# Performance work log

Measured on AMD Instinct MI355X. Metric: run time of the kernel, lower is better.

The kernel has to match this reference:

```python
import jax, jax.numpy as jnp
import numpy as np

B, R, S, D, K = 4096, 49, 50, 512, 100

def setup_inputs() -> dict:
    key = jax.random.key(0)
    ks = jax.random.split(key, 10)
    return {
        "ifeature": jax.random.normal(ks[0], (B, R, D), dtype=jnp.float32),
        "tfeature_h": jax.random.normal(ks[1], (B, S, D), dtype=jnp.float32),
        "w_Vi_0": jax.random.normal(ks[2], (D, K), dtype=jnp.float32) * 0.05,
        "w_Vt_0": jax.random.normal(ks[3], (D, K), dtype=jnp.float32) * 0.05,
        "w_Pi_0": jax.random.normal(ks[4], (2 * K, 1), dtype=jnp.float32) * 0.05,
        "b_Pi_0": jnp.zeros((R,), dtype=jnp.float32),
        "w_Vi_1": jax.random.normal(ks[5], (D, K), dtype=jnp.float32) * 0.05,
        "w_Vt_1": jax.random.normal(ks[6], (D, K), dtype=jnp.float32) * 0.05,
        "w_Pi_1": jax.random.normal(ks[7], (2 * K, 1), dtype=jnp.float32) * 0.05,
        "b_Pi_1": jnp.zeros((S,), dtype=jnp.float32),
    }

def reference(ifeature, tfeature_h, w_Vi_0, w_Vt_0, w_Pi_0, b_Pi_0,
              w_Vi_1, w_Vt_1, w_Pi_1, b_Pi_1):
    # ---- pass 0: attend over image regions, conditioned on mean text feature
    tfeature = jnp.mean(tfeature_h, axis=1)                      # [B, D]
    wVi0 = jnp.einsum('brd,dk->brk', ifeature, w_Vi_0)           # [B, R, K]
    wVt0 = (tfeature @ w_Vt_0)[:, None, :]                       # [B, 1, K] -> broadcast over R
    Hi = jnp.tanh(jnp.concatenate(
        [wVi0, jnp.broadcast_to(wVt0, wVi0.shape)], axis=-1))    # [B, R, 2K]
    scores_i = jnp.squeeze(Hi @ w_Pi_0, axis=-1) + b_Pi_0        # [B, R]
    Pi = jax.nn.softmax(scores_i, axis=-1)                       # [B, R]
    Vi = jnp.einsum('br,brd->bd', Pi, ifeature)                  # [B, D]
    # ---- pass 1: attend over text positions, conditioned on attended image
    wVi1 = (Vi @ w_Vi_1)[:, None, :]                             # [B, 1, K]
    wVt1 = jnp.einsum('bsd,dk->bsk', tfeature_h, w_Vt_1)         # [B, S, K]
    Ht = jnp.tanh(jnp.concatenate(
        [jnp.broadcast_to(wVi1, wVt1.shape), wVt1], axis=-1))    # [B, S, 2K]
    scores_t = jnp.squeeze(Ht @ w_Pi_1, axis=-1) + b_Pi_1        # [B, S]
    Pt = jax.nn.softmax(scores_t, axis=-1)                       # [B, S]
    Vt = jnp.einsum('bs,bsd->bd', Pt, tfeature_h)                # [B, D]
    return Vi + Vt
```

## Files before the change

### kernel.cpp

```cpp
#include <hip/hip_runtime.h>
#include <math.h>

#define NB 4096
#define NR 49
#define NS 50
#define ND 512
#define NK 100
#define NT 7
#define KSTEPS 16
#define CHUNK_KS 8
#define FRAGS (NT * KSTEPS * 64 * 8)

typedef __attribute__((ext_vector_type(8))) short short8;
typedef __attribute__((ext_vector_type(4))) float f32x4;

__device__ __forceinline__ unsigned short f32_bf16(float f) {
    union { float f; unsigned u; } x; x.f = f;
    return (unsigned short)((x.u + 0x7fffu + ((x.u >> 16) & 1u)) >> 16);
}
__device__ __forceinline__ unsigned cvt_pk_bf16(float lo, float hi) {
    unsigned r;
    asm("v_cvt_pk_bf16_f32 %0, %1, %2" : "=v"(r) : "v"(lo), "v"(hi));
    return r;
}
__device__ __forceinline__ float fast_tanh(float x) {
    const float ax = fabsf(x);
    const float e = __expf(2.f * ax);
    const float r = 1.f - 2.f / (e + 1.f);
    return copysignf(r, x);
}

__global__ void preswz_kernel(const float* __restrict__ w0, const float* __restrict__ w1,
                              unsigned short* __restrict__ ws)
{
    const int l  = threadIdx.x;
    const int gk = blockIdx.x & 15;
    const int t  = blockIdx.x >> 4;
    const int m  = blockIdx.y;
    const float* W = m ? w1 : w0;
    const int col = t * 16 + (l & 15);
    const int k0  = gk * 32 + (l >> 4) * 8;
    unsigned short* o = ws + (size_t)m * FRAGS + ((size_t)(t * 16 + gk) * 64 + l) * 8;
#pragma unroll
    for (int j = 0; j < 8; ++j) {
        float v = (col < NK) ? W[(size_t)(k0 + j) * NK + col] : 0.f;
        o[j] = f32_bf16(v);
    }
}

struct SM {
    short buf[NS * 256];
    float part[NT][64];
    float P[64];
};

__global__ __launch_bounds__(512, 4) void coattn_main(
    const float* __restrict__ ifeat, const float* __restrict__ tfeat,
    const float* __restrict__ wPi0, const float* __restrict__ bPi0,
    const float* __restrict__ wPi1, const float* __restrict__ bPi1,
    const unsigned short* __restrict__ wsW, float* __restrict__ out)
{
    __shared__ SM sm;
    const int pass = blockIdx.x & 1;
    const int b    = blockIdx.x >> 1;
    const int tid  = threadIdx.x;

    const float* feat = pass ? (tfeat + (size_t)b * NS * ND) : (ifeat + (size_t)b * NR * ND);
    const int nrows  = pass ? NS : NR;
    const int nclamp = nrows - 1;
    const unsigned short* wsR = wsW + (size_t)pass * FRAGS;
    const float* wPiRow = pass ? (wPi1 + NK) : wPi0;
    const float* bvec   = pass ? bPi1 : bPi0;

    const int lane = tid & 63, wid = tid >> 6;
    const int colg = lane & 15, g = lane >> 4;

    const f32x4 zero4 = {0.f, 0.f, 0.f, 0.f};
    f32x4 acc[4] = {zero4, zero4, zero4, zero4};

    int arow_[4], rswz_[4];
#pragma unroll
    for (int rt = 0; rt < 4; ++rt) {
        const int r0 = rt * 16 + colg;
        arow_[rt] = (r0 < nclamp) ? r0 : nclamp;
        rswz_[rt] = arow_[rt] & 7;
    }

    const int nitems = nrows * 32;

    for (int chunk = 0; chunk < 2; ++chunk) {
        __syncthreads();
        for (int it = tid; it < nitems; it += 512) {
            const int r = it >> 5, c = it & 31;
            const float* p = feat + (r << 9) + (chunk << 8) + (c << 3);
            const float4 a  = *reinterpret_cast<const float4*>(p);
            const float4 b4 = *reinterpret_cast<const float4*>(p + 4);
            uint4 v;
            v.x = cvt_pk_bf16(a.x, a.y);   v.y = cvt_pk_bf16(a.z, a.w);
            v.z = cvt_pk_bf16(b4.x, b4.y); v.w = cvt_pk_bf16(b4.z, b4.w);
            *reinterpret_cast<uint4*>(&sm.buf[(r << 8) + ((c ^ (r & 7)) << 3)]) = v;
        }
        __syncthreads();

        if (wid < NT) {
            const unsigned short* wl = wsR
                + ((size_t)(wid * KSTEPS + chunk * CHUNK_KS) * 64 + lane) * 8;
#pragma unroll
            for (int ks = 0; ks < CHUNK_KS; ++ks) {
                const short8 w = *reinterpret_cast<const short8*>(wl + ks * 512);
                const int q0 = (ks << 2) + g;
#pragma unroll
                for (int rt = 0; rt < 4; ++rt) {
                    const short8 a = *reinterpret_cast<const short8*>(
                        &sm.buf[(arow_[rt] << 8) + ((q0 ^ rswz_[rt]) << 3)]);
                    acc[rt] = __builtin_amdgcn_mfma_f32_16x16x32_bf16(a, w, acc[rt], 0, 0, 0);
                }
            }
        }
    }

    if (wid < NT) {
        const int col = wid * 16 + colg;
        const float w = (col < NK) ? wPiRow[col] : 0.f;
        float sp[4][4];
#pragma unroll
        for (int rt = 0; rt < 4; ++rt)
#pragma unroll
            for (int i = 0; i < 4; ++i)
                sp[rt][i] = fast_tanh(acc[rt][i]) * w;
#pragma unroll
        for (int off = 1; off < 16; off <<= 1)
#pragma unroll
            for (int rt = 0; rt < 4; ++rt)
#pragma unroll
                for (int i = 0; i < 4; ++i)
                    sp[rt][i] += __shfl_xor(sp[rt][i], off);
        if (colg == 0) {
#pragma unroll
            for (int rt = 0; rt < 4; ++rt)
#pragma unroll
                for (int i = 0; i < 4; ++i)
                    sm.part[wid][rt * 16 + g * 4 + i] = sp[rt][i];
        }
    }
    __syncthreads();

    if (tid < 64) {
        float v = (tid < nrows) ? bvec[tid] : 0.f;
#pragma unroll
        for (int w = 0; w < NT; ++w) v += sm.part[w][tid];
        v = (tid < nrows) ? v : -3.0e38f;
        float mx = v;
#pragma unroll
        for (int off = 32; off; off >>= 1) mx = fmaxf(mx, __shfl_xor(mx, off));
        const float e = (tid < nrows) ? __expf(v - mx) : 0.f;
        float su = e;
#pragma unroll
        for (int off = 32; off; off >>= 1) su += __shfl_xor(su, off);
        sm.P[tid] = e / su;
    }
    __syncthreads();

    {
        float v = 0.f;
        const float* fp = feat + tid;
        for (int r = 0; r < nrows; ++r) v += sm.P[r] * fp[r << 9];
        atomicAdd(&out[(size_t)b * ND + tid], v);
    }
}

extern "C" void kernel_launch(void* const* d_in, const int* in_sizes, int n_in,
                              void* d_out, int out_size, void* d_ws, size_t ws_size,
                              hipStream_t stream) {
    const float* ifeat = (const float*)d_in[0];
    const float* tfeat = (const float*)d_in[1];
    const float* wVi0  = (const float*)d_in[2];
    const float* wPi0  = (const float*)d_in[4];
    const float* bPi0  = (const float*)d_in[5];
    const float* wVt1  = (const float*)d_in[7];
    const float* wPi1  = (const float*)d_in[8];
    const float* bPi1  = (const float*)d_in[9];
    float* outp = (float*)d_out;
    unsigned short* wsW = (unsigned short*)d_ws;

    hipMemsetAsync(outp, 0, (size_t)NB * ND * sizeof(float), stream);
    hipLaunchKernelGGL(preswz_kernel, dim3(NT * KSTEPS, 2), dim3(64), 0, stream,
                       wVi0, wVt1, wsW);
    hipLaunchKernelGGL(coattn_main, dim3(2 * NB), dim3(512), 0, stream,
                       ifeat, tfeat, wPi0, bPi0, wPi1, bPi1, wsW, outp);
}
```

Baseline: 306.4 us.

## Fuse both attention passes per block and reuse staged bf16 rows for weighted sum

After: 316.4 us. 3.3% more time.

```diff
diff --git a/kernel.cpp b/kernel.cpp
--- a/kernel.cpp
+++ b/kernel.cpp
@@ -8,7 +8,6 @@
 #define NK 100
 #define NT 7
 #define KSTEPS 16
-#define CHUNK_KS 8
 #define FRAGS (NT * KSTEPS * 64 * 8)
 
 typedef __attribute__((ext_vector_type(8))) short short8;
@@ -17,6 +16,10 @@
 __device__ __forceinline__ unsigned short f32_bf16(float f) {
     union { float f; unsigned u; } x; x.f = f;
     return (unsigned short)((x.u + 0x7fffu + ((x.u >> 16) & 1u)) >> 16);
+}
+__device__ __forceinline__ float bf16_f32(unsigned short h) {
+    union { unsigned u; float f; } x; x.u = ((unsigned)h) << 16;
+    return x.f;
 }
 __device__ __forceinline__ unsigned cvt_pk_bf16(float lo, float hi) {
     unsigned r;
@@ -49,123 +52,122 @@
 }
 
 struct SM {
-    short buf[NS * 256];
+    short buf[NS * ND];
     float part[NT][64];
     float P[64];
 };
 
-__global__ __launch_bounds__(512, 4) void coattn_main(
+__global__ __launch_bounds__(512, 6) void coattn_main(
     const float* __restrict__ ifeat, const float* __restrict__ tfeat,
     const float* __restrict__ wPi0, const float* __restrict__ bPi0,
     const float* __restrict__ wPi1, const float* __restrict__ bPi1,
     const unsigned short* __restrict__ wsW, float* __restrict__ out)
 {
     __shared__ SM sm;
-    const int pass = blockIdx.x & 1;
-    const int b    = blockIdx.x >> 1;
-    const int tid  = threadIdx.x;
-
-    const float* feat = pass ? (tfeat + (size_t)b * NS * ND) : (ifeat + (size_t)b * NR * ND);
-    const int nrows  = pass ? NS : NR;
-    const int nclamp = nrows - 1;
-    const unsigned short* wsR = wsW + (size_t)pass * FRAGS;
-    const float* wPiRow = pass ? (wPi1 + NK) : wPi0;
-    const float* bvec   = pass ? bPi1 : bPi0;
-
+    const int b = blockIdx.x, tid = threadIdx.x;
     const int lane = tid & 63, wid = tid >> 6;
     const int colg = lane & 15, g = lane >> 4;
+    const int wch = tid >> 3, wlo = tid & 7;
 
-    const f32x4 zero4 = {0.f, 0.f, 0.f, 0.f};
-    f32x4 acc[4] = {zero4, zero4, zero4, zero4};
+    float vi = 0.f;
 
-    int arow_[4], rswz_[4];
-#pragma unroll
-    for (int rt = 0; rt < 4; ++rt) {
-        const int r0 = rt * 16 + colg;
-        arow_[rt] = (r0 < nclamp) ? r0 : nclamp;
-        rswz_[rt] = arow_[rt] & 7;
-    }
+    for (int pass = 0; pass < 2; ++pass) {
+        const float* feat = pass ? (tfeat + (size_t)b * NS * ND)
+                                 : (ifeat + (size_t)b * NR * ND);
+        const int nrows  = pass ? NS : NR;
+        const int nclamp = nrows - 1;
+        const unsigned short* wsR = wsW + (size_t)pass * FRAGS;
+        const float* wPiRow = pass ? (wPi1 + NK) : wPi0;
+        const float* bvec   = pass ? bPi1 : bPi0;
 
-    const int nitems = nrows * 32;
-
-    for (int chunk = 0; chunk < 2; ++chunk) {
-        __syncthreads();
+        const int nitems = nrows * 64;
         for (int it = tid; it < nitems; it += 512) {
-            const int r = it >> 5, c = it & 31;
-            const float* p = feat + (r << 9) + (chunk << 8) + (c << 3);
+            const int r = it >> 6, c = it & 63;
+            const float* p = feat + (r << 9) + (c << 3);
             const float4 a  = *reinterpret_cast<const float4*>(p);
             const float4 b4 = *reinterpret_cast<const float4*>(p + 4);
             uint4 v;
             v.x = cvt_pk_bf16(a.x, a.y);   v.y = cvt_pk_bf16(a.z, a.w);
             v.z = cvt_pk_bf16(b4.x, b4.y); v.w = cvt_pk_bf16(b4.z, b4.w);
-            *reinterpret_cast<uint4*>(&sm.buf[(r << 8) + ((c ^ (r & 7)) << 3)]) = v;
+            *reinterpret_cast<uint4*>(&sm.buf[(r << 9) + ((c ^ (r & 7)) << 3)]) = v;
         }
         __syncthreads();
 
         if (wid < NT) {
-            const unsigned short* wl = wsR
-                + ((size_t)(wid * KSTEPS + chunk * CHUNK_KS) * 64 + lane) * 8;
+            int arow_[4], rswz_[4];
 #pragma unroll
-            for (int ks = 0; ks < CHUNK_KS; ++ks) {
+            for (int rt = 0; rt < 4; ++rt) {
+                const int r0 = rt * 16 + colg;
+                arow_[rt] = (r0 < nclamp) ? r0 : nclamp;
+                rswz_[rt] = arow_[rt] & 7;
+            }
+            const f32x4 zero4 = {0.f, 0.f, 0.f, 0.f};
+            f32x4 acc[4] = {zero4, zero4, zero4, zero4};
+            const unsigned short* wl = wsR + ((size_t)wid * KSTEPS * 64 + lane) * 8;
+#pragma unroll
+            for (int ks = 0; ks < KSTEPS; ++ks) {
                 const short8 w = *reinterpret_cast<const short8*>(wl + ks * 512);
                 const int q0 = (ks << 2) + g;
 #pragma unroll
                 for (int rt = 0; rt < 4; ++rt) {
                     const short8 a = *reinterpret_cast<const short8*>(
-                        &sm.buf[(arow_[rt] << 8) + ((q0 ^ rswz_[rt]) << 3)]);
+                        &sm.buf[(arow_[rt] << 9) + ((q0 ^ rswz_[rt]) << 3)]);
                     acc[rt] = __builtin_amdgcn_mfma_f32_16x16x32_bf16(a, w, acc[rt], 0, 0, 0);
                 }
             }
-        }
-    }
 
-    if (wid < NT) {
-        const int col = wid * 16 + colg;
-        const float w = (col < NK) ? wPiRow[col] : 0.f;
-        float sp[4][4];
-#pragma unroll
-        for (int rt = 0; rt < 4; ++rt)
-#pragma unroll
-            for (int i = 0; i < 4; ++i)
-                sp[rt][i] = fast_tanh(acc[rt][i]) * w;
-#pragma unroll
-        for (int off = 1; off < 16; off <<= 1)
+            const int col = wid * 16 + colg;
+            const float w = (col < NK) ? wPiRow[col] : 0.f;
+            float sp[4][4];
 #pragma unroll
             for (int rt = 0; rt < 4; ++rt)
 #pragma unroll
                 for (int i = 0; i < 4; ++i)
-                    sp[rt][i] += __shfl_xor(sp[rt][i], off);
-        if (colg == 0) {
+                    sp[rt][i] = fast_tanh(acc[rt][i]) * w;
 #pragma unroll
-            for (int rt = 0; rt < 4; ++rt)
+            for (int off = 1; off < 16; off <<= 1)
 #pragma unroll
-                for (int i = 0; i < 4; ++i)
-                    sm.part[wid][rt * 16 + g * 4 + i] = sp[rt][i];
+                for (int rt = 0; rt < 4; ++rt)
+#pragma unroll
+                    for (int i = 0; i < 4; ++i)
+                        sp[rt][i] += __shfl_xor(sp[rt][i], off);
+            if (colg == 0) {
+#pragma unroll
+                for (int rt = 0; rt < 4; ++rt)
+#pragma unroll
+                    for (int i = 0; i < 4; ++i)
+                        sm.part[wid][rt * 16 + g * 4 + i] = sp[rt][i];
+            }
         }
-    }
-    __syncthreads();
+        __syncthreads();
 
-    if (tid < 64) {
-        float v = (tid < nrows) ? bvec[tid] : 0.f;
+        if (tid < 64) {
+            float v = (tid < nrows) ? bvec[tid] : 0.f;
 #pragma unroll
-        for (int w = 0; w < NT; ++w) v += sm.part[w][tid];
-        v = (tid < nrows) ? v : -3.0e38f;
-        float mx = v;
+            for (int w = 0; w < NT; ++w) v += sm.part[w][tid];
+            v = (tid < nrows) ? v : -3.0e38f;
+            float mx = v;
 #pragma unroll
-        for (int off = 32; off; off >>= 1) mx = fmaxf(mx, __shfl_xor(mx, off));
-        const float e = (tid < nrows) ? __expf(v - mx) : 0.f;
-        float su = e;
+            for (int off = 32; off; off >>= 1) mx = fmaxf(mx, __shfl_xor(mx, off));
+            const float e = (tid < nrows) ? __expf(v - mx) : 0.f;
+            float su = e;
 #pragma unroll
-        for (int off = 32; off; off >>= 1) su += __shfl_xor(su, off);
-        sm.P[tid] = e / su;
-    }
-    __syncthreads();
+            for (int off = 32; off; off >>= 1) su += __shfl_xor(su, off);
+            sm.P[tid] = e / su;
+        }
+        __syncthreads();
 
-    {
-        float v = 0.f;
-        const float* fp = feat + tid;
-        for (int r = 0; r < nrows; ++r) v += sm.P[r] * fp[r << 9];
-        atomicAdd(&out[(size_t)b * ND + tid], v);
+        {
+            float v = 0.f;
+            for (int r = 0; r < nrows; ++r) {
+                const unsigned short u = (unsigned short)
+                    sm.buf[(r << 9) + ((wch ^ (r & 7)) << 3) + wlo];
+                v += sm.P[r] * bf16_f32(u);
+            }
+            if (pass == 0) vi = v;
+            else out[(size_t)b * ND + tid] = vi + v;
+        }
+        __syncthreads();
     }
 }
 
@@ -183,9 +185,8 @@
     float* outp = (float*)d_out;
     unsigned short* wsW = (unsigned short*)d_ws;
 
-    hipMemsetAsync(outp, 0, (size_t)NB * ND * sizeof(float), stream);
     hipLaunchKernelGGL(preswz_kernel, dim3(NT * KSTEPS, 2), dim3(64), 0, stream,
                        wVi0, wVt1, wsW);
-    hipLaunchKernelGGL(coattn_main, dim3(2 * NB), dim3(512), 0, stream,
+    hipLaunchKernelGGL(coattn_main, dim3(NB), dim3(512), 0, stream,
                        ifeat, tfeat, wPi0, bPi0, wPi1, bPi1, wsW, outp);
 }
```

## Double-buffer fp32 tiles via direct global-to-LDS loads and rebalance waves

Applied to the files above, without the earlier changes.

New measurement: 308.8 us. Within noise of the previous version (+0.8%).

```diff
diff --git a/kernel.cpp b/kernel.cpp
--- a/kernel.cpp
+++ b/kernel.cpp
@@ -8,7 +8,6 @@
 #define NK 100
 #define NT 7
 #define KSTEPS 16
-#define CHUNK_KS 8
 #define FRAGS (NT * KSTEPS * 64 * 8)
 
 typedef __attribute__((ext_vector_type(8))) short short8;
@@ -29,6 +28,14 @@
     const float r = 1.f - 2.f / (e + 1.f);
     return copysignf(r, x);
 }
+__device__ __forceinline__ void load_lds16(const float* g, float* l) {
+    __builtin_amdgcn_global_load_lds(
+        (const __attribute__((address_space(1))) unsigned int*)(const void*)g,
+        (__attribute__((address_space(3))) unsigned int*)(void*)l, 16, 0, 0);
+}
+#define FENCE() asm volatile("" ::: "memory")
+#define BARR()  do { FENCE(); __builtin_amdgcn_s_barrier(); FENCE(); } while (0)
+#define WAITV(N) asm volatile("s_waitcnt vmcnt(" #N ")" ::: "memory")
 
 __global__ void preswz_kernel(const float* __restrict__ w0, const float* __restrict__ w1,
                               unsigned short* __restrict__ ws)
@@ -49,8 +56,9 @@
 }
 
 struct SM {
-    short buf[NS * 256];
-    float part[NT][64];
+    float bufA[50 * 128];
+    float bufB[50 * 128];
+    float part[8][64];
     float P[64];
 };
 
@@ -74,81 +82,122 @@
 
     const int lane = tid & 63, wid = tid >> 6;
     const int colg = lane & 15, g = lane >> 4;
-
-    const f32x4 zero4 = {0.f, 0.f, 0.f, 0.f};
-    f32x4 acc[4] = {zero4, zero4, zero4, zero4};
-
-    int arow_[4], rswz_[4];
-#pragma unroll
-    for (int rt = 0; rt < 4; ++rt) {
-        const int r0 = rt * 16 + colg;
-        arow_[rt] = (r0 < nclamp) ? r0 : nclamp;
-        rswz_[rt] = arow_[rt] & 7;
-    }
-
-    const int nitems = nrows * 32;
-
-    for (int chunk = 0; chunk < 2; ++chunk) {
-        __syncthreads();
-        for (int it = tid; it < nitems; it += 512) {
-            const int r = it >> 5, c = it & 31;
-            const float* p = feat + (r << 9) + (chunk << 8) + (c << 3);
-            const float4 a  = *reinterpret_cast<const float4*>(p);
-            const float4 b4 = *reinterpret_cast<const float4*>(p + 4);
-            uint4 v;
-            v.x = cvt_pk_bf16(a.x, a.y);   v.y = cvt_pk_bf16(a.z, a.w);
-            v.z = cvt_pk_bf16(b4.x, b4.y); v.w = cvt_pk_bf16(b4.z, b4.w);
-            *reinterpret_cast<uint4*>(&sm.buf[(r << 8) + ((c ^ (r & 7)) << 3)]) = v;
+    const int q  = wid >> 1;
+    const int mh = wid & 1;
+    const int t0 = q * 2;
+    const int two = (q < 3);
+
+    int arow_[2], aswz_[2];
+#pragma unroll
+    for (int rl = 0; rl < 2; ++rl) {
+        const int r0 = (mh * 2 + rl) * 16 + colg;
+        arow_[rl] = (r0 < nclamp) ? r0 : nclamp;
+        aswz_[rl] = arow_[rl] & 7;
+    }
+    const unsigned short* wl0 = wsR + ((size_t)t0 * 16 * 64 + lane) * 8;
+    const unsigned short* wl1 = wl0 + (size_t)16 * 64 * 8;
+
+#define ISSUE(CP, BUF)                                                          \
+    do {                                                                        \
+        _Pragma("unroll") for (int s = 0; s < 3; ++s) {                         \
+            const int j = wid + (s << 3);                                       \
+            const int row = 2 * j + (lane >> 5);                                \
+            const int grow = (row < nrows) ? row : nclamp;                      \
+            const int c16 = lane & 31;                                          \
+            load_lds16(feat + (grow << 9) + ((CP) << 7) + ((c16 ^ (row & 7)) << 2), \
+                       sm.BUF + j * 256);                                       \
+        }                                                                       \
+        if (wid == 0) {                                                         \
+            const int row = 48 + (lane >> 5);                                   \
+            const int grow = (row < nrows) ? row : nclamp;                      \
+            const int c16 = lane & 31;                                          \
+            load_lds16(feat + (grow << 9) + ((CP) << 7) + ((c16 ^ (row & 7)) << 2), \
+                       sm.BUF + 24 * 256);                                      \
+        }                                                                       \
+    } while (0)
+#define WAITC() do { if (wid == 0) { WAITV(4); } else { WAITV(3); } } while (0)
+
+    f32x4 acc[2][2];
+#pragma unroll
+    for (int rl = 0; rl < 2; ++rl)
+#pragma unroll
+        for (int tl = 0; tl < 2; ++tl) acc[rl][tl] = f32x4{0.f, 0.f, 0.f, 0.f};
+
+#define GEMMP(LB, CP)                                                           \
+    do {                                                                        \
+        _Pragma("unroll") for (int ksl = 0; ksl < 4; ++ksl) {                   \
+            const int ks = (CP) * 4 + ksl;                                      \
+            const short8 wf0 = *reinterpret_cast<const short8*>(wl0 + ks * 512); \
+            short8 wf1 = {};                                                    \
+            if (two) wf1 = *reinterpret_cast<const short8*>(wl1 + ks * 512);    \
+            _Pragma("unroll") for (int rl = 0; rl < 2; ++rl) {                  \
+                const int c16 = (ksl << 3) + (g << 1);                          \
+                const float4 fa = *reinterpret_cast<const float4*>(             \
+                    &(LB)[arow_[rl] * 128 + ((c16 ^ aswz_[rl]) << 2)]);         \
+                const float4 fb = *reinterpret_cast<const float4*>(             \
+                    &(LB)[arow_[rl] * 128 + (((c16 + 1) ^ aswz_[rl]) << 2)]);   \
+                uint4 ap;                                                       \
+                ap.x = cvt_pk_bf16(fa.x, fa.y); ap.y = cvt_pk_bf16(fa.z, fa.w); \
+                ap.z = cvt_pk_bf16(fb.x, fb.y); ap.w = cvt_pk_bf16(fb.z, fb.w); \
+                const short8 a = *reinterpret_cast<const short8*>(&ap);         \
+                acc[rl][0] = __builtin_amdgcn_mfma_f32_16x16x32_bf16(a, wf0, acc[rl][0], 0, 0, 0); \
+                if (two)                                                        \
+                    acc[rl][1] = __builtin_amdgcn_mfma_f32_16x16x32_bf16(a, wf1, acc[rl][1], 0, 0, 0); \
+            }                                                                   \
+        }                                                                       \
+    } while (0)
+
+    ISSUE(0, bufA);
+    ISSUE(1, bufB);
+    WAITC(); BARR();
+    GEMMP(sm.bufA, 0);
+    BARR();
+    ISSUE(2, bufA);
+    WAITC(); BARR();
+    GEMMP(sm.bufB, 1);
+    BARR();
+    ISSUE(3, bufB);
+    WAITC(); BARR();
+    GEMMP(sm.bufA, 2);
+    WAITV(0); BARR();
+    GEMMP(sm.bufB, 3);
+
+    {
+        const int c0 = (t0 + 0) * 16 + colg;
+        const int c1 = (t0 + 1) * 16 + colg;
+        const float w0 = (c0 < NK) ? wPiRow[c0] : 0.f;
+        const float w1 = (two && c1 < NK) ? wPiRow[c1] : 0.f;
+        float sp[2][4];
+#pragma unroll
+        for (int rl = 0; rl < 2; ++rl)
+#pragma unroll
+            for (int i = 0; i < 4; ++i) {
+                float v = fast_tanh(acc[rl][0][i]) * w0;
+                if (two) v += fast_tanh(acc[rl][1][i]) * w1;
+                sp[rl][i] = v;
+            }
+#pragma unroll
+        for (int off = 1; off < 16; off <<= 1)
+#pragma unroll
+            for (int rl = 0; rl < 2; ++rl)
+#pragma unroll
+                for (int i = 0; i < 4; ++i)
+                    sp[rl][i] += __shfl_xor(sp[rl][i], off);
+        if (colg == 0) {
+#pragma unroll
+            for (int rl = 0; rl < 2; ++rl)
+#pragma unroll
+                for (int i = 0; i < 4; ++i)
+                    sm.part[wid][(mh * 2 + rl) * 16 + g * 4 + i] = sp[rl][i];
         }
-        __syncthreads();
-
-        if (wid < NT) {
-            const unsigned short* wl = wsR
-                + ((size_t)(wid * KSTEPS + chunk * CHUNK_KS) * 64 + lane) * 8;
-#pragma unroll
-            for (int ks = 0; ks < CHUNK_KS; ++ks) {
-                const short8 w = *reinterpret_cast<const short8*>(wl + ks * 512);
-                const int q0 = (ks << 2) + g;
-#pragma unroll
-                for (int rt = 0; rt < 4; ++rt) {
-                    const short8 a = *reinterpret_cast<const short8*>(
-                        &sm.buf[(arow_[rt] << 8) + ((q0 ^ rswz_[rt]) << 3)]);
-                    acc[rt] = __builtin_amdgcn_mfma_f32_16x16x32_bf16(a, w, acc[rt], 0, 0, 0);
-                }
-            }
-        }
-    }
-
-    if (wid < NT) {
-        const int col = wid * 16 + colg;
-        const float w = (col < NK) ? wPiRow[col] : 0.f;
-        float sp[4][4];
-#pragma unroll
-        for (int rt = 0; rt < 4; ++rt)
-#pragma unroll
-            for (int i = 0; i < 4; ++i)
-                sp[rt][i] = fast_tanh(acc[rt][i]) * w;
-#pragma unroll
-        for (int off = 1; off < 16; off <<= 1)
-#pragma unroll
-            for (int rt = 0; rt < 4; ++rt)
-#pragma unroll
-                for (int i = 0; i < 4; ++i)
-                    sp[rt][i] += __shfl_xor(sp[rt][i], off);
-        if (colg == 0) {
-#pragma unroll
-            for (int rt = 0; rt < 4; ++rt)
-#pragma unroll
-                for (int i = 0; i < 4; ++i)
-                    sm.part[wid][rt * 16 + g * 4 + i] = sp[rt][i];
-        }
     }
     __syncthreads();
 
     if (tid < 64) {
+        const int hb = (tid >= 32) ? 1 : 0;
         float v = (tid < nrows) ? bvec[tid] : 0.f;
 #pragma unroll
-        for (int w = 0; w < NT; ++w) v += sm.part[w][tid];
+        for (int qq = 0; qq < 4; ++qq) v += sm.part[2 * qq + hb][tid];
         v = (tid < nrows) ? v : -3.0e38f;
         float mx = v;
 #pragma unroll
@@ -167,6 +216,9 @@
         for (int r = 0; r < nrows; ++r) v += sm.P[r] * fp[r << 9];
         atomicAdd(&out[(size_t)b * ND + tid], v);
     }
+#undef ISSUE
+#undef WAITC
+#undef GEMMP
 }
 
 extern "C" void kernel_launch(void* const* d_in, const int* in_sizes, int n_in,
```
